# Kernel optimization log

Hardware: AMD Instinct MI355X
Metric: run time of the kernel (lower is better)

Reference implementation:

```python
import jax, jax.numpy as jnp
import numpy as np

VOCAB, T, IN, H, L = 32000, 4096, 512, 256, 2


def setup_inputs() -> dict:
    key = jax.random.key(0)
    ks = jax.random.split(key, 32)
    inp = {}
    inp["tokens"] = jax.random.randint(ks[0], (T,), 0, VOCAB)
    inp["emb"] = jax.random.normal(ks[1], (VOCAB, IN), dtype=jnp.float32) * 0.02
    i = 2
    for d in ("f", "b"):
        for l in range(L):
            in_l = IN if l == 0 else H
            inp[f"{d}_Wih{l}"] = jax.random.normal(ks[i], (4 * H, in_l), dtype=jnp.float32) * 0.05; i += 1
            inp[f"{d}_Whh{l}"] = jax.random.normal(ks[i], (4 * H, H), dtype=jnp.float32) * 0.05; i += 1
            inp[f"{d}_bih{l}"] = jnp.zeros((4 * H,), dtype=jnp.float32)
            inp[f"{d}_bhh{l}"] = jnp.zeros((4 * H,), dtype=jnp.float32)
    return inp


def _lstm_layer(x_seq, Wih, Whh, bih, bhh):
    # x_seq: [T, in]; torch.nn.LSTMCell gate order: i, f, g, o
    Hh = Whh.shape[1]
    b = bih + bhh
    def step(carry, x):
        h, c = carry
        g = x @ Wih.T + h @ Whh.T + b           # [4H]
        i_, f_, g_, o_ = jnp.split(g, 4)
        c = jax.nn.sigmoid(f_) * c + jax.nn.sigmoid(i_) * jnp.tanh(g_)
        h = jax.nn.sigmoid(o_) * jnp.tanh(c)
        return (h, c), h
    z = jnp.zeros((Hh,), x_seq.dtype)
    (h, c), hs = jax.lax.scan(step, (z, z), x_seq)
    return hs, h, c                              # [T,H], [H], [H]


def _run_dir(x_seq, params):
    finals = []
    h_seq = x_seq
    for (Wih, Whh, bih, bhh) in params:
        h_seq, h, c = _lstm_layer(h_seq, Wih, Whh, bih, bhh)
        finals.append((c, h))
    return h_seq, finals


def reference(tokens, emb,
              f_Wih0, f_Whh0, f_bih0, f_bhh0, f_Wih1, f_Whh1, f_bih1, f_bhh1,
              b_Wih0, b_Whh0, b_bih0, b_bhh0, b_Wih1, b_Whh1, b_bih1, b_bhh1):
    x = emb[tokens]                              # [T, IN] embedding lookup
    fparams = [(f_Wih0, f_Whh0, f_bih0, f_bhh0), (f_Wih1, f_Whh1, f_bih1, f_bhh1)]
    bparams = [(b_Wih0, b_Whh0, b_bih0, b_bhh0), (b_Wih1, b_Whh1, b_bih1, b_bhh1)]
    f_out, f_fin = _run_dir(x, fparams)          # forward over sequence
    b_out_rev, b_fin = _run_dir(x[::-1], bparams)  # backward over reversed sequence
    b_out = b_out_rev[::-1]
    outputs = jnp.concatenate([f_out, b_out], axis=-1)  # [T, 2H]
    cell_memories = jnp.stack([jnp.stack([f_fin[l][0], b_fin[l][0]]) for l in range(L)])  # [L,2,H]
    hidden_states = jnp.stack([jnp.stack([f_fin[l][1], b_fin[l][1]]) for l in range(L)])  # [L,2,H]
    return cell_memories, hidden_states, outputs
```

## Files before the change

### kernel.cpp

```cpp
#include <hip/hip_runtime.h>
#include <math.h>

#define T_SEQ 4096

__device__ __forceinline__ float sigmoidf_(float x) {
  return 1.0f / (1.0f + expf(-x));
}

__device__ __forceinline__ unsigned long long pack_h(int tag, float h) {
  return ((unsigned long long)(unsigned)tag << 32) |
         (unsigned long long)__float_as_uint(h);
}

__device__ __forceinline__ void st_pub(unsigned long long* p, unsigned long long v) {
  asm volatile("global_store_dwordx2 %0, %1, off sc0 sc1"
               :: "v"(p), "v"(v) : "memory");
}

__device__ __forceinline__ float poll_h(const unsigned long long* p, unsigned want) {
  for (;;) {
    unsigned long long a, b;
    asm volatile("global_load_dwordx2 %0, %2, off sc0 sc1\n\t"
                 "global_load_dwordx2 %1, %2, off sc0 sc1\n\t"
                 "s_waitcnt vmcnt(1)"
                 : "=&v"(a), "=&v"(b) : "v"(p) : "memory");
    if ((unsigned)(a >> 32) == want) {
      asm volatile("s_waitcnt vmcnt(0)" ::: "memory");
      return __uint_as_float((unsigned)a);
    }
    asm volatile("s_waitcnt vmcnt(0)" ::: "memory");
    if ((unsigned)(b >> 32) == want) return __uint_as_float((unsigned)b);
  }
}

__global__ void gather_emb(const int* __restrict__ tokens,
                           const float4* __restrict__ emb4,
                           float4* __restrict__ X4) {
  int i = blockIdx.x * 256 + threadIdx.x;
  int t = i >> 7;
  int q = i & 127;
  X4[i] = emb4[(long)tokens[t] * 128 + q];
}

__global__ __launch_bounds__(256) void gemm_proj(
    const float* __restrict__ Xf, const float* __restrict__ Xb, int revb,
    const float* __restrict__ Wf, const float* __restrict__ Wb,
    const float* __restrict__ bihf, const float* __restrict__ bhhf,
    const float* __restrict__ bihb, const float* __restrict__ bhhb,
    float* __restrict__ Pf, float* __restrict__ Pb, int K)
{
  const int dirb = blockIdx.z;
  const float* X  = dirb ? Xb : Xf;
  const float* W  = dirb ? Wb : Wf;
  const float* bih = dirb ? bihb : bihf;
  const float* bhh = dirb ? bhhb : bhhf;
  float* Pp = dirb ? Pb : Pf;
  const int rev = dirb ? revb : 0;

  const int bn = blockIdx.x;
  const int bm = blockIdx.y;
  const int tid = threadIdx.x;
  const int tx = tid & 15, ty = tid >> 4;

  __shared__ float Xs[16][68];
  __shared__ float Ws[16][68];

  float acc[4][4] = {{0.f}};

  const int lrow = tid >> 2;
  const int lk4  = (tid & 3) * 4;
  const int xrow = bm * 64 + lrow;
  const int xsrc = rev ? (4095 - xrow) : xrow;
  const float* xptr = X + (long)xsrc * K + lk4;
  const float* wptr = W + (long)(bn * 64 + lrow) * K + lk4;

  for (int k0 = 0; k0 < K; k0 += 16) {
    float4 xv = *(const float4*)(xptr + k0);
    float4 wv = *(const float4*)(wptr + k0);
    __syncthreads();
    Xs[lk4 + 0][lrow] = xv.x; Xs[lk4 + 1][lrow] = xv.y;
    Xs[lk4 + 2][lrow] = xv.z; Xs[lk4 + 3][lrow] = xv.w;
    Ws[lk4 + 0][lrow] = wv.x; Ws[lk4 + 1][lrow] = wv.y;
    Ws[lk4 + 2][lrow] = wv.z; Ws[lk4 + 3][lrow] = wv.w;
    __syncthreads();
    #pragma unroll
    for (int kk = 0; kk < 16; ++kk) {
      float4 a = *(const float4*)(&Xs[kk][ty * 4]);
      float4 b = *(const float4*)(&Ws[kk][tx * 4]);
      acc[0][0] = fmaf(a.x, b.x, acc[0][0]); acc[0][1] = fmaf(a.x, b.y, acc[0][1]);
      acc[0][2] = fmaf(a.x, b.z, acc[0][2]); acc[0][3] = fmaf(a.x, b.w, acc[0][3]);
      acc[1][0] = fmaf(a.y, b.x, acc[1][0]); acc[1][1] = fmaf(a.y, b.y, acc[1][1]);
      acc[1][2] = fmaf(a.y, b.z, acc[1][2]); acc[1][3] = fmaf(a.y, b.w, acc[1][3]);
      acc[2][0] = fmaf(a.z, b.x, acc[2][0]); acc[2][1] = fmaf(a.z, b.y, acc[2][1]);
      acc[2][2] = fmaf(a.z, b.z, acc[2][2]); acc[2][3] = fmaf(a.z, b.w, acc[2][3]);
      acc[3][0] = fmaf(a.w, b.x, acc[3][0]); acc[3][1] = fmaf(a.w, b.y, acc[3][1]);
      acc[3][2] = fmaf(a.w, b.z, acc[3][2]); acc[3][3] = fmaf(a.w, b.w, acc[3][3]);
    }
  }

  const int c0 = bn * 64 + tx * 4;
  #pragma unroll
  for (int i = 0; i < 4; ++i) {
    const int r = bm * 64 + ty * 4 + i;
    float4 o4;
    o4.x = acc[i][0] + bih[c0 + 0] + bhh[c0 + 0];
    o4.y = acc[i][1] + bih[c0 + 1] + bhh[c0 + 1];
    o4.z = acc[i][2] + bih[c0 + 2] + bhh[c0 + 2];
    o4.w = acc[i][3] + bih[c0 + 3] + bhh[c0 + 3];
    *(float4*)(&Pp[(long)r * 1024 + c0]) = o4;
  }
}

__global__ __launch_bounds__(512, 2) void lstm_fused(
    const float* __restrict__ P0f, const float* __restrict__ P0b,
    const float* __restrict__ Whh0f, const float* __restrict__ Whh0b,
    const float* __restrict__ Wih1f, const float* __restrict__ Whh1f,
    const float* __restrict__ bih1f, const float* __restrict__ bhh1f,
    const float* __restrict__ Wih1b, const float* __restrict__ Whh1b,
    const float* __restrict__ bih1b, const float* __restrict__ bhh1b,
    float* __restrict__ out,
    unsigned long long* __restrict__ ring0,
    unsigned long long* __restrict__ h1x)
{
  const int bx = blockIdx.x;
  const int t  = threadIdx.x;

  __shared__ float hx[512];
  __shared__ float part[8 * 264];
  __shared__ float gact[256];
  __shared__ float lds_c[64];

  if (t < 64) lds_c[t] = 0.0f;

  if (bx < 8) {
    const int d = bx >> 2, w = bx & 3;
    const float* __restrict__ P = d ? P0b : P0f;
    const float* __restrict__ W = d ? Whh0b : Whh0f;
    unsigned long long* ring = ring0 + (long)d * T_SEQ * 256;

    const int kb = t >> 6;
    const int jg = t & 63;

    float wreg[128];
    #pragma unroll
    for (int jj = 0; jj < 4; ++jj) {
      const int m = jg * 4 + jj;
      const int j = (m >> 6) * 256 + w * 64 + (m & 63);
      const float4* wrow = (const float4*)(W + (long)j * 256 + kb * 32);
      #pragma unroll
      for (int kq = 0; kq < 8; ++kq) {
        float4 v = wrow[kq];
        wreg[jj * 32 + kq * 4 + 0] = v.x;
        wreg[jj * 32 + kq * 4 + 1] = v.y;
        wreg[jj * 32 + kq * 4 + 2] = v.z;
        wreg[jj * 32 + kq * 4 + 3] = v.w;
      }
    }

    const long pj   = (long)((t >> 6) * 256 + w * 64 + (t & 63));
    const int  cell = w * 64 + (t & 63);

    for (int s = 0; s < T_SEQ; ++s) {
      float pval = 0.0f;
      if (t < 256) pval = P[(long)s * 1024 + pj];

      if (s == 0) {
        if (t < 256) hx[t] = 0.0f;
      } else if (t < 256) {
        hx[t] = poll_h(ring + (long)(s - 1) * 256 + t, (unsigned)s);
      }
      __syncthreads();

      float a0 = 0.f, a1 = 0.f, a2 = 0.f, a3 = 0.f;
      const float4* h4 = (const float4*)&hx[kb * 32];
      #pragma unroll
      for (int kq = 0; kq < 8; ++kq) {
        float4 hv = h4[kq];
        a0 = fmaf(wreg[0 * 32 + kq * 4 + 0], hv.x, a0);
        a0 = fmaf(wreg[0 * 32 + kq * 4 + 1], hv.y, a0);
        a0 = fmaf(wreg[0 * 32 + kq * 4 + 2], hv.z, a0);
        a0 = fmaf(wreg[0 * 32 + kq * 4 + 3], hv.w, a0);
        a1 = fmaf(wreg[1 * 32 + kq * 4 + 0], hv.x, a1);
        a1 = fmaf(wreg[1 * 32 + kq * 4 + 1], hv.y, a1);
        a1 = fmaf(wreg[1 * 32 + kq * 4 + 2], hv.z, a1);
        a1 = fmaf(wreg[1 * 32 + kq * 4 + 3], hv.w, a1);
        a2 = fmaf(wreg[2 * 32 + kq * 4 + 0], hv.x, a2);
        a2 = fmaf(wreg[2 * 32 + kq * 4 + 1], hv.y, a2);
        a2 = fmaf(wreg[2 * 32 + kq * 4 + 2], hv.z, a2);
        a2 = fmaf(wreg[2 * 32 + kq * 4 + 3], hv.w, a2);
        a3 = fmaf(wreg[3 * 32 + kq * 4 + 0], hv.x, a3);
        a3 = fmaf(wreg[3 * 32 + kq * 4 + 1], hv.y, a3);
        a3 = fmaf(wreg[3 * 32 + kq * 4 + 2], hv.z, a3);
        a3 = fmaf(wreg[3 * 32 + kq * 4 + 3], hv.w, a3);
      }
      float4 av; av.x = a0; av.y = a1; av.z = a2; av.w = a3;
      *(float4*)(&part[kb * 264 + jg * 4]) = av;
      __syncthreads();

      if (t < 256) {
        float g = pval;
        #pragma unroll
        for (int q = 0; q < 8; ++q) g += part[q * 264 + t];
        gact[t] = ((t >> 6) == 2) ? tanhf(g) : sigmoidf_(g);
      }
      __syncthreads();

      if (t < 64) {
        float c = gact[64 + t] * lds_c[t] + gact[t] * gact[128 + t];
        float h = gact[192 + t] * tanhf(c);
        lds_c[t] = c;
        st_pub(ring + (long)s * 256 + cell, pack_h(s + 1, h));
        if (s == T_SEQ - 1) {
          out[d * 256 + cell] = c;
          out[1024 + d * 256 + cell] = h;
        }
      }
    }
  } else {
    const int i1 = bx - 8, d = i1 >> 3, w1 = i1 & 7;
    const float* __restrict__ Wih = d ? Wih1b : Wih1f;
    const float* __restrict__ Whh = d ? Whh1b : Whh1f;
    const float* __restrict__ bih = d ? bih1b : bih1f;
    const float* __restrict__ bhh = d ? bhh1b : bhh1f;
    unsigned long long* ring = ring0 + (long)d * T_SEQ * 256;
    unsigned long long* slot = h1x + d * 512;
    float* hout = d ? (out + 2048 + (long)4095 * 512 + 256) : (out + 2048);
    const long hstr = d ? -512 : 512;

    const int kb = t >> 6;
    const int jg = t & 63;

    float wreg[2][64];
    #pragma unroll
    for (int rr = 0; rr < 2; ++rr) {
      const int m = jg * 2 + rr;
      const int j = (m >> 5) * 256 + w1 * 32 + (m & 31);
      const float* srcw = (kb < 4) ? (Wih + (long)j * 256 + kb * 64)
                                   : (Whh + (long)j * 256 + (kb - 4) * 64);
      const float4* s4 = (const float4*)srcw;
      #pragma unroll
      for (int q = 0; q < 16; ++q) {
        float4 v = s4[q];
        wreg[rr][q * 4 + 0] = v.x; wreg[rr][q * 4 + 1] = v.y;
        wreg[rr][q * 4 + 2] = v.z; wreg[rr][q * 4 + 3] = v.w;
      }
    }

    const int cell = w1 * 32 + (t & 31);
    float bsum = 0.0f;
    if (t < 128) {
      const int j = (t >> 5) * 256 + w1 * 32 + (t & 31);
      bsum = bih[j] + bhh[j];
    }

    for (int s = 0; s < T_SEQ; ++s) {
      if (t < 256) {
        hx[t] = poll_h(ring + (long)s * 256 + t, (unsigned)(s + 1));
      } else {
        hx[t] = poll_h(slot + ((s + 1) & 1) * 256 + (t - 256), (unsigned)s);
      }
      __syncthreads();

      float a0 = 0.f, a1 = 0.f;
      const float4* h4 = (const float4*)&hx[kb * 64];
      #pragma unroll
      for (int q = 0; q < 16; ++q) {
        float4 hv = h4[q];
        a0 = fmaf(wreg[0][q * 4 + 0], hv.x, a0);
        a0 = fmaf(wreg[0][q * 4 + 1], hv.y, a0);
        a0 = fmaf(wreg[0][q * 4 + 2], hv.z, a0);
        a0 = fmaf(wreg[0][q * 4 + 3], hv.w, a0);
        a1 = fmaf(wreg[1][q * 4 + 0], hv.x, a1);
        a1 = fmaf(wreg[1][q * 4 + 1], hv.y, a1);
        a1 = fmaf(wreg[1][q * 4 + 2], hv.z, a1);
        a1 = fmaf(wreg[1][q * 4 + 3], hv.w, a1);
      }
      float2 av2; av2.x = a0; av2.y = a1;
      *(float2*)(&part[kb * 264 + jg * 2]) = av2;
      __syncthreads();

      if (t < 128) {
        float g = bsum;
        #pragma unroll
        for (int q = 0; q < 8; ++q) g += part[q * 264 + t];
        gact[t] = ((t >> 5) == 2) ? tanhf(g) : sigmoidf_(g);
      }
      __syncthreads();

      if (t < 32) {
        float c = gact[32 + t] * lds_c[t] + gact[t] * gact[64 + t];
        float h = gact[96 + t] * tanhf(c);
        lds_c[t] = c;
        st_pub(&slot[(s & 1) * 256 + cell], pack_h(s + 1, h));
        hout[(long)s * hstr + cell] = h;
        if (s == T_SEQ - 1) {
          out[512 + d * 256 + cell] = c;
          out[1024 + 512 + d * 256 + cell] = h;
        }
      }
    }
  }
}

extern "C" void kernel_launch(void* const* d_in, const int* in_sizes, int n_in,
                              void* d_out, int out_size, void* d_ws, size_t ws_size,
                              hipStream_t stream) {
  const int*   tokens = (const int*)d_in[0];
  const float* emb    = (const float*)d_in[1];
  const float* fWih0 = (const float*)d_in[2];
  const float* fWhh0 = (const float*)d_in[3];
  const float* fbih0 = (const float*)d_in[4];
  const float* fbhh0 = (const float*)d_in[5];
  const float* fWih1 = (const float*)d_in[6];
  const float* fWhh1 = (const float*)d_in[7];
  const float* fbih1 = (const float*)d_in[8];
  const float* fbhh1 = (const float*)d_in[9];
  const float* bWih0 = (const float*)d_in[10];
  const float* bWhh0 = (const float*)d_in[11];
  const float* bbih0 = (const float*)d_in[12];
  const float* bbhh0 = (const float*)d_in[13];
  const float* bWih1 = (const float*)d_in[14];
  const float* bWhh1 = (const float*)d_in[15];
  const float* bbih1 = (const float*)d_in[16];
  const float* bbhh1 = (const float*)d_in[17];

  float* out = (float*)d_out;
  float* ws  = (float*)d_ws;

  float* X   = ws;
  float* P0f = ws + 4194304;
  float* P0b = ws + 8388608;
  unsigned long long* ring0 = (unsigned long long*)ws;
  unsigned long long* h1x   = (unsigned long long*)(ws + 12582912);

  gather_emb<<<2048, 256, 0, stream>>>(tokens, (const float4*)emb, (float4*)X);

  gemm_proj<<<dim3(16, 64, 2), 256, 0, stream>>>(
      X, X, 1, fWih0, bWih0, fbih0, fbhh0, bbih0, bbhh0, P0f, P0b, 512);

  hipMemsetAsync(ring0, 0, (size_t)2 * T_SEQ * 256 * sizeof(unsigned long long), stream);
  hipMemsetAsync(h1x, 0, 1024 * sizeof(unsigned long long), stream);

  lstm_fused<<<dim3(24), 512, 0, stream>>>(
      P0f, P0b, fWhh0, bWhh0,
      fWih1, fWhh1, fbih1, fbhh1,
      bWih1, bWhh1, bbih1, bbhh1,
      out, ring0, h1x);
}
```

Before: 7.346 ms.

## Place all LSTM blocks of a direction on one XCD and poll with L2-scoped loads

The persistent LSTM kernel now launches 96 blocks and keeps only those whose index mod 8 is 0 or 1. Under round-robin block-to-XCD dispatch, this should put every block of a direction on the same XCD. Handoff polling mostly uses sc0 loads that can hit the shared L2, with an occasional sc0 sc1 load as a fallback. Stores are issued twice, once at each scope. The goal is lower cross-block synchronisation latency per timestep, but it depends on an undocumented dispatch order and the visibility of sc0-only traffic.

```diff
diff --git a/kernel.cpp b/kernel.cpp
--- a/kernel.cpp
+++ b/kernel.cpp
@@ -12,24 +12,29 @@
          (unsigned long long)__float_as_uint(h);
 }
 
+__device__ __forceinline__ unsigned long long ld_sc0(const unsigned long long* p) {
+  unsigned long long v;
+  asm volatile("global_load_dwordx2 %0, %1, off sc0\n\ts_waitcnt vmcnt(0)"
+               : "=v"(v) : "v"(p) : "memory");
+  return v;
+}
+__device__ __forceinline__ unsigned long long ld_mall(const unsigned long long* p) {
+  unsigned long long v;
+  asm volatile("global_load_dwordx2 %0, %1, off sc0 sc1\n\ts_waitcnt vmcnt(0)"
+               : "=v"(v) : "v"(p) : "memory");
+  return v;
+}
 __device__ __forceinline__ void st_pub(unsigned long long* p, unsigned long long v) {
-  asm volatile("global_store_dwordx2 %0, %1, off sc0 sc1"
+  asm volatile("global_store_dwordx2 %0, %1, off sc0\n\t"
+               "global_store_dwordx2 %0, %1, off sc0 sc1"
                :: "v"(p), "v"(v) : "memory");
 }
-
 __device__ __forceinline__ float poll_h(const unsigned long long* p, unsigned want) {
+  int it = 0;
   for (;;) {
-    unsigned long long a, b;
-    asm volatile("global_load_dwordx2 %0, %2, off sc0 sc1\n\t"
-                 "global_load_dwordx2 %1, %2, off sc0 sc1\n\t"
-                 "s_waitcnt vmcnt(1)"
-                 : "=&v"(a), "=&v"(b) : "v"(p) : "memory");
-    if ((unsigned)(a >> 32) == want) {
-      asm volatile("s_waitcnt vmcnt(0)" ::: "memory");
-      return __uint_as_float((unsigned)a);
-    }
-    asm volatile("s_waitcnt vmcnt(0)" ::: "memory");
-    if ((unsigned)(b >> 32) == want) return __uint_as_float((unsigned)b);
+    unsigned long long v = ((it & 3) == 3) ? ld_mall(p) : ld_sc0(p);
+    if ((unsigned)(v >> 32) == want) return __uint_as_float((unsigned)v);
+    ++it;
   }
 }
 
@@ -125,6 +130,11 @@
   const int bx = blockIdx.x;
   const int t  = threadIdx.x;
 
+  const int lane8 = bx & 7;
+  if (lane8 > 1) return;
+  const int d   = lane8;
+  const int sub = bx >> 3;
+
   __shared__ float hx[512];
   __shared__ float part[8 * 264];
   __shared__ float gact[256];
@@ -132,11 +142,12 @@
 
   if (t < 64) lds_c[t] = 0.0f;
 
-  if (bx < 8) {
-    const int d = bx >> 2, w = bx & 3;
+  unsigned long long* ring = ring0 + (long)d * T_SEQ * 256;
+
+  if (sub < 4) {
+    const int w = sub;
     const float* __restrict__ P = d ? P0b : P0f;
     const float* __restrict__ W = d ? Whh0b : Whh0f;
-    unsigned long long* ring = ring0 + (long)d * T_SEQ * 256;
 
     const int kb = t >> 6;
     const int jg = t & 63;
@@ -217,12 +228,11 @@
       }
     }
   } else {
-    const int i1 = bx - 8, d = i1 >> 3, w1 = i1 & 7;
+    const int w1 = sub - 4;
     const float* __restrict__ Wih = d ? Wih1b : Wih1f;
     const float* __restrict__ Whh = d ? Whh1b : Whh1f;
     const float* __restrict__ bih = d ? bih1b : bih1f;
     const float* __restrict__ bhh = d ? bhh1b : bhh1f;
-    unsigned long long* ring = ring0 + (long)d * T_SEQ * 256;
     unsigned long long* slot = h1x + d * 512;
     float* hout = d ? (out + 2048 + (long)4095 * 512 + 256) : (out + 2048);
     const long hstr = d ? -512 : 512;
@@ -341,7 +351,7 @@
   hipMemsetAsync(ring0, 0, (size_t)2 * T_SEQ * 256 * sizeof(unsigned long long), stream);
   hipMemsetAsync(h1x, 0, 1024 * sizeof(unsigned long long), stream);
 
-  lstm_fused<<<dim3(24), 512, 0, stream>>>(
+  lstm_fused<<<dim3(96), 512, 0, stream>>>(
       P0f, P0b, fWhh0, bWhh0,
       fWih1, fWhh1, fbih1, fbhh1,
       bWih1, bWhh1, bbih1, bbhh1,
```

After: 6.663 ms. 9.3% less time.

## Replicate h broadcasts into per-consumer mailboxes with 16-slot rings and paired polling

Applied to the files above, without the earlier changes.

Each producer block now writes its h values into a private 16-slot ring per consumer block, plus the archive ring. Consumers poll their own mailbox with 16-byte loads that read two values at once, and fall back to the archive when the slot has already been overwritten. Blocks keep their own h slice locally in LDS instead of polling for it, and half the polling threads sleep briefly to cut memory traffic. The aim is to reduce contention and latency in the cross-block handoff on the serial critical path, at the cost of 12 or 8 extra stores per produced value.

```diff
diff --git a/kernel.cpp b/kernel.cpp
--- a/kernel.cpp
+++ b/kernel.cpp
@@ -3,33 +3,55 @@
 
 #define T_SEQ 4096
 
+typedef unsigned long long u64;
+typedef unsigned int v4u __attribute__((ext_vector_type(4)));
+
 __device__ __forceinline__ float sigmoidf_(float x) {
   return 1.0f / (1.0f + expf(-x));
 }
 
-__device__ __forceinline__ unsigned long long pack_h(int tag, float h) {
-  return ((unsigned long long)(unsigned)tag << 32) |
-         (unsigned long long)__float_as_uint(h);
-}
-
-__device__ __forceinline__ void st_pub(unsigned long long* p, unsigned long long v) {
+__device__ __forceinline__ u64 pack_h(int tag, float h) {
+  return ((u64)(unsigned)tag << 32) | (u64)__float_as_uint(h);
+}
+
+__device__ __forceinline__ v4u probe16(const u64* p) {
+  v4u v;
+  asm volatile("global_load_dwordx4 %0, %1, off sc0 sc1\n\ts_waitcnt vmcnt(0)"
+               : "=v"(v) : "v"(p) : "memory");
+  return v;
+}
+__device__ __forceinline__ void st_mall(u64* p, u64 v) {
   asm volatile("global_store_dwordx2 %0, %1, off sc0 sc1"
                :: "v"(p), "v"(v) : "memory");
 }
-
-__device__ __forceinline__ float poll_h(const unsigned long long* p, unsigned want) {
+__device__ __forceinline__ void half_rt_sleep() {
+  asm volatile("s_sleep 7" ::: "memory");
+}
+
+__device__ __forceinline__ void poll2(const u64* pvt, const u64* arch,
+                                      unsigned want, float* d0, float* d1) {
   for (;;) {
-    unsigned long long a, b;
-    asm volatile("global_load_dwordx2 %0, %2, off sc0 sc1\n\t"
-                 "global_load_dwordx2 %1, %2, off sc0 sc1\n\t"
-                 "s_waitcnt vmcnt(1)"
-                 : "=&v"(a), "=&v"(b) : "v"(p) : "memory");
-    if ((unsigned)(a >> 32) == want) {
-      asm volatile("s_waitcnt vmcnt(0)" ::: "memory");
-      return __uint_as_float((unsigned)a);
-    }
-    asm volatile("s_waitcnt vmcnt(0)" ::: "memory");
-    if ((unsigned)(b >> 32) == want) return __uint_as_float((unsigned)b);
+    v4u v = probe16(pvt);
+    if (v[1] == want && v[3] == want) {
+      *d0 = __uint_as_float(v[0]); *d1 = __uint_as_float(v[2]); return;
+    }
+    if (v[1] > want || v[3] > want) {
+      for (;;) {
+        v4u a = probe16(arch);
+        if (a[1] == want && a[3] == want) {
+          *d0 = __uint_as_float(a[0]); *d1 = __uint_as_float(a[2]); return;
+        }
+      }
+    }
+  }
+}
+__device__ __forceinline__ void poll2n(const u64* pvt, unsigned want,
+                                       float* d0, float* d1) {
+  for (;;) {
+    v4u v = probe16(pvt);
+    if (v[1] == want && v[3] == want) {
+      *d0 = __uint_as_float(v[0]); *d1 = __uint_as_float(v[2]); return;
+    }
   }
 }
 
@@ -119,8 +141,9 @@
     const float* __restrict__ Wih1b, const float* __restrict__ Whh1b,
     const float* __restrict__ bih1b, const float* __restrict__ bhh1b,
     float* __restrict__ out,
-    unsigned long long* __restrict__ ring0,
-    unsigned long long* __restrict__ h1x)
+    u64* __restrict__ ring0,
+    u64* __restrict__ pvt0,
+    u64* __restrict__ pvt1)
 {
   const int bx = blockIdx.x;
   const int t  = threadIdx.x;
@@ -136,7 +159,9 @@
     const int d = bx >> 2, w = bx & 3;
     const float* __restrict__ P = d ? P0b : P0f;
     const float* __restrict__ W = d ? Whh0b : Whh0f;
-    unsigned long long* ring = ring0 + (long)d * T_SEQ * 256;
+    u64* arch  = ring0 + (long)d * T_SEQ * 256;
+    u64* pvtd  = pvt0 + (long)d * 12 * 16 * 256;
+    const u64* mybuf = pvtd + (long)w * 16 * 256;
 
     const int kb = t >> 6;
     const int jg = t & 63;
@@ -167,7 +192,14 @@
       if (s == 0) {
         if (t < 256) hx[t] = 0.0f;
       } else if (t < 256) {
-        hx[t] = poll_h(ring + (long)(s - 1) * 256 + t, (unsigned)s);
+        const int i = t & 127;
+        const int wi = i * 2;
+        if ((wi >> 6) != w) {
+          if (t >= 128) half_rt_sleep();
+          const int slot = (s - 1) & 15;
+          poll2(mybuf + slot * 256 + wi, arch + (long)(s - 1) * 256 + wi,
+                (unsigned)s, &hx[wi], &hx[wi + 1]);
+        }
       }
       __syncthreads();
 
@@ -209,7 +241,13 @@
         float c = gact[64 + t] * lds_c[t] + gact[t] * gact[128 + t];
         float h = gact[192 + t] * tanhf(c);
         lds_c[t] = c;
-        st_pub(ring + (long)s * 256 + cell, pack_h(s + 1, h));
+        hx[cell] = h;
+        const u64 pk = pack_h(s + 1, h);
+        u64* base = pvtd + (long)(s & 15) * 256 + cell;
+        #pragma unroll
+        for (int cns = 0; cns < 12; ++cns)
+          st_mall(base + (long)cns * 4096, pk);
+        st_mall(arch + (long)s * 256 + cell, pk);
         if (s == T_SEQ - 1) {
           out[d * 256 + cell] = c;
           out[1024 + d * 256 + cell] = h;
@@ -222,8 +260,10 @@
     const float* __restrict__ Whh = d ? Whh1b : Whh1f;
     const float* __restrict__ bih = d ? bih1b : bih1f;
     const float* __restrict__ bhh = d ? bhh1b : bhh1f;
-    unsigned long long* ring = ring0 + (long)d * T_SEQ * 256;
-    unsigned long long* slot = h1x + d * 512;
+    u64* arch = ring0 + (long)d * T_SEQ * 256;
+    const u64* myh0 = pvt0 + (long)(d * 12 + 4 + w1) * 16 * 256;
+    u64* pvt1d = pvt1 + (long)d * 8 * 16 * 256;
+    const u64* myh1 = pvt1d + (long)w1 * 16 * 256;
     float* hout = d ? (out + 2048 + (long)4095 * 512 + 256) : (out + 2048);
     const long hstr = d ? -512 : 512;
 
@@ -255,9 +295,21 @@
 
     for (int s = 0; s < T_SEQ; ++s) {
       if (t < 256) {
-        hx[t] = poll_h(ring + (long)s * 256 + t, (unsigned)(s + 1));
+        const int i = t & 127;
+        const int wi = i * 2;
+        if (t >= 128) half_rt_sleep();
+        poll2(myh0 + (long)(s & 15) * 256 + wi, arch + (long)s * 256 + wi,
+              (unsigned)(s + 1), &hx[wi], &hx[wi + 1]);
       } else {
-        hx[t] = poll_h(slot + ((s + 1) & 1) * 256 + (t - 256), (unsigned)s);
+        const int i = (t - 256) & 127;
+        const int wi = i * 2;
+        if (s == 0) {
+          hx[256 + wi] = 0.0f; hx[257 + wi] = 0.0f;
+        } else if ((wi >> 5) != w1) {
+          if (t >= 384) half_rt_sleep();
+          poll2n(myh1 + (long)((s - 1) & 15) * 256 + wi, (unsigned)s,
+                 &hx[256 + wi], &hx[257 + wi]);
+        }
       }
       __syncthreads();
 
@@ -291,7 +343,12 @@
         float c = gact[32 + t] * lds_c[t] + gact[t] * gact[64 + t];
         float h = gact[96 + t] * tanhf(c);
         lds_c[t] = c;
-        st_pub(&slot[(s & 1) * 256 + cell], pack_h(s + 1, h));
+        hx[256 + cell] = h;
+        const u64 pk = pack_h(s + 1, h);
+        u64* base = pvt1d + (long)(s & 15) * 256 + cell;
+        #pragma unroll
+        for (int cns = 0; cns < 8; ++cns)
+          st_mall(base + (long)cns * 4096, pk);
         hout[(long)s * hstr + cell] = h;
         if (s == T_SEQ - 1) {
           out[512 + d * 256 + cell] = c;
@@ -330,20 +387,21 @@
   float* X   = ws;
   float* P0f = ws + 4194304;
   float* P0b = ws + 8388608;
-  unsigned long long* ring0 = (unsigned long long*)ws;
-  unsigned long long* h1x   = (unsigned long long*)(ws + 12582912);
+  u64* ring0 = (u64*)ws;
+  u64* pvt0  = (u64*)(ws + 12582912);
+  u64* pvt1  = (u64*)(ws + 12779520);
 
   gather_emb<<<2048, 256, 0, stream>>>(tokens, (const float4*)emb, (float4*)X);
 
   gemm_proj<<<dim3(16, 64, 2), 256, 0, stream>>>(
       X, X, 1, fWih0, bWih0, fbih0, fbhh0, bbih0, bbhh0, P0f, P0b, 512);
 
-  hipMemsetAsync(ring0, 0, (size_t)2 * T_SEQ * 256 * sizeof(unsigned long long), stream);
-  hipMemsetAsync(h1x, 0, 1024 * sizeof(unsigned long long), stream);
+  hipMemsetAsync(ring0, 0, (size_t)2 * T_SEQ * 256 * sizeof(u64), stream);
+  hipMemsetAsync(pvt0, 0, (size_t)(98304 + 65536) * sizeof(u64), stream);
 
   lstm_fused<<<dim3(24), 512, 0, stream>>>(
       P0f, P0b, fWhh0, bWhh0,
       fWih1, fWhh1, fbih1, fbhh1,
       bWih1, bWhh1, bbih1, bbhh1,
-      out, ring0, h1x);
-}
+      out, ring0, pvt0, pvt1);
+}
```

New measurement: 7.888 ms. 7.4% more time.
